# Kernel tuning notes

Hardware: AMD Instinct MI355X
Metric: run time of the kernel (lower is better)

Reference implementation:

```python
import jax, jax.numpy as jnp
import numpy as np

N_QUBITS = 12
N_LAYERS = 6
BATCH = 512
DIM = 2 ** N_QUBITS


def _apply_1q(psi, G, wire):
    """Apply a single-qubit gate on `wire` (wire 0 = most significant).
    psi: [B, 2^n] complex. G: [2,2] (shared) or [B,2,2] (batched)."""
    B = psi.shape[0]
    left = 2 ** wire
    psi = psi.reshape(B, left, 2, -1)
    if G.ndim == 2:
        psi = jnp.einsum('ij,bxjy->bxiy', G, psi)
    else:
        psi = jnp.einsum('bij,bxjy->bxiy', G, psi)
    return psi.reshape(B, -1)


def _apply_cnot(psi, c, t):
    """CNOT with control c, target t on [B, 2^n] state."""
    B = psi.shape[0]
    ps = psi.reshape((B,) + (2,) * N_QUBITS)
    ca, ta = c + 1, t + 1
    c0 = jnp.take(ps, 0, axis=ca)
    c1 = jnp.take(ps, 1, axis=ca)
    flip_ax = ta if ta < ca else ta - 1
    c1 = jnp.flip(c1, axis=flip_ax)  # X on target within control=1 block
    ps = jnp.stack([c0, c1], axis=ca)
    return ps.reshape(B, -1)


def _circuit(x, weights):
    B = x.shape[0]
    psi = jnp.zeros((B, DIM), jnp.complex64).at[:, 0].set(1.0)

    # AngleEmbedding: RY(x_w) on each wire (batched gate matrices)
    h = 0.5 * x
    c, s = jnp.cos(h).astype(jnp.complex64), jnp.sin(h).astype(jnp.complex64)
    for w in range(N_QUBITS):
        G = jnp.stack([jnp.stack([c[:, w], -s[:, w]], -1),
                       jnp.stack([s[:, w], c[:, w]], -1)], -2)  # [B,2,2]
        psi = _apply_1q(psi, G, w)

    # StronglyEntanglingLayers: Rot(phi,theta,omega) per wire, then ring of CNOTs
    for l in range(N_LAYERS):
        phi, theta, omega = weights[l, :, 0], weights[l, :, 1], weights[l, :, 2]
        ct = jnp.cos(0.5 * theta).astype(jnp.complex64)
        st = jnp.sin(0.5 * theta).astype(jnp.complex64)
        ep = jnp.exp(-0.5j * (phi + omega).astype(jnp.complex64))
        em = jnp.exp(0.5j * (phi - omega).astype(jnp.complex64))
        # Rot = RZ(omega) RY(theta) RZ(phi)
        m00 = ep * ct
        m01 = -em * st
        m10 = jnp.conj(em) * st
        m11 = jnp.conj(ep) * ct
        for w in range(N_QUBITS):
            G = jnp.array([[m00[w], m01[w]], [m10[w], m11[w]]], jnp.complex64)
            psi = _apply_1q(psi, G, w)
        r = l % (N_QUBITS - 1) + 1
        for w in range(N_QUBITS):
            psi = _apply_cnot(psi, w, (w + r) % N_QUBITS)

    # <Z_w> for every wire
    probs = psi.real ** 2 + psi.imag ** 2  # [B, 2^n]
    exps = []
    for w in range(N_QUBITS):
        p = probs.reshape(B, 2 ** w, 2, -1)
        exps.append(p[:, :, 0, :].sum((1, 2)) - p[:, :, 1, :].sum((1, 2)))
    return jnp.stack(exps, -1)  # [B, n_qubits]


def setup_inputs() -> dict:
    key = jax.random.key(0)
    k1, k2, k3, k4 = jax.random.split(key, 4)
    x = jax.random.uniform(k1, (BATCH, N_QUBITS), jnp.float32, -np.pi, np.pi)
    weights = jax.random.uniform(k2, (N_LAYERS, N_QUBITS, 3), jnp.float32, 0.0, 2.0 * np.pi)
    W = jax.random.normal(k3, (1, N_QUBITS), jnp.float32) * 0.3
    b = jax.random.normal(k4, (1,), jnp.float32) * 0.01
    return {"x": x, "weights": weights, "W": W, "b": b}


def reference(x, weights, W, b):
    z = _circuit(x, weights)              # [B, n_qubits]
    y = z @ W.T + b                       # [B, 1]
    return y.squeeze(-1)                  # [B]
```

## Files before the change

kernel.cpp:

```cpp
#include <hip/hip_runtime.h>
#include <stdint.h>

#define NQ 12
#define DIM 4096
#define NLAYERS 6
#define TPB 512
#define NL 8

typedef float v2f __attribute__((ext_vector_type(2)));

struct Pass_t {
    uint32_t WT[9];
    uint32_t WL[NL];
    uint32_t RT[9];
    uint32_t RL[NL];
};
struct CK_t {
    Pass_t PS1, PS2, PS3;
    Pass_t P1[NLAYERS];
    uint32_t frow[NQ];
};

constexpr uint32_t S1f(uint32_t k){ return ((k&7u)<<3) | ((k>>3)&7u) | (k & 0xFC0u); }
constexpr uint32_t S2f(uint32_t k){ return ((k&7u)<<6) | (k & 0x38u) | ((k>>6)&7u) | (k & 0xE00u); }
constexpr uint32_t S3f(uint32_t k){ return ((k&7u)<<9) | (k & 0x1F8u) | ((k>>9)&7u); }

constexpr uint32_t ech_reduce(const uint32_t* v, int n, uint32_t x){
    bool ch = true;
    while (ch) {
        ch = false;
        for (int i = 0; i < n; i++)
            if (v[i] && (x ^ v[i]) < x) { x ^= v[i]; ch = true; }
    }
    return x;
}

constexpr Pass_t build_pass(const uint32_t* Mc) {
    Pass_t P{};
    uint32_t rows[12]{}; int nr = 0;
    {
        uint32_t e1[4]{}, e2[4]{}; int n1 = 0, n2 = 0;
        for (int step = 0; step < 4; step++) {
            bool found = false;
            for (int pc = 1; pc <= 3 && !found; pc++) {
                for (int a = 0; a < 12 && !found; a++)
                for (int b = (pc >= 2 ? a + 1 : 12); (pc >= 2 ? b < 12 : b == 12) && !found; b++)
                for (int c = (pc == 3 ? b + 1 : 12); (pc == 3 ? c < 12 : c == 12) && !found; c++) {
                    uint32_t m = (1u << a);
                    if (pc >= 2) m |= (1u << b);
                    if (pc == 3) m |= (1u << c);
                    uint32_t v1 = (m >> 3) & 15u;
                    uint32_t v2 = 0;
                    for (int j = 0; j < 4; j++)
                        v2 |= (uint32_t)(__builtin_popcount(m & Mc[3 + j]) & 1) << j;
                    uint32_t r1 = ech_reduce(e1, n1, v1);
                    uint32_t r2 = ech_reduce(e2, n2, v2);
                    if (r1 && r2) {
                        rows[nr++] = m; e1[n1++] = r1; e2[n2++] = r2; found = true;
                    }
                }
            }
            if (!found) { rows[nr] = 1u << (3 + nr); nr++; }
        }
    }
    {
        uint32_t ef[12]{}; int nf = 0;
        for (int i = 0; i < nr; i++) {
            uint32_t r = ech_reduce(ef, nf, rows[i]);
            if (r) ef[nf++] = r;
        }
        for (uint32_t m = 1; m < 4096u && nr < 12; m++) {
            uint32_t r = ech_reduce(ef, nf, m);
            if (r) { rows[nr++] = m; ef[nf++] = r; }
        }
    }
    uint32_t col[12]{}, rc[12]{};
    for (int j = 0; j < 12; j++) {
        uint32_t c = 0;
        for (int i = 0; i < 12; i++) c |= (uint32_t)((rows[i] >> j) & 1u) << i;
        col[j] = c;
    }
    for (int j = 0; j < 12; j++) {
        uint32_t a = 0, mc = Mc[j];
        for (int q = 0; q < 12; q++) if ((mc >> q) & 1u) a ^= col[q];
        rc[j] = a;
    }
    for (int j = 0; j < 9; j++) { P.WT[j] = col[3 + j]; P.RT[j] = rc[3 + j]; }
    for (int l = 0; l < NL; l++) {
        uint32_t aw = 0, ar = 0;
        for (int q = 0; q < 3; q++) if ((l >> q) & 1) { aw ^= col[q]; ar ^= rc[q]; }
        P.WL[l] = aw; P.RL[l] = ar;
    }
    return P;
}

constexpr CK_t build_ck() {
    CK_t ck{};
    uint32_t Acols[NLAYERS][NQ]{}, Aicol5[NQ]{};
    for (int l = 0; l < NLAYERS; l++) {
        int r = l % (NQ - 1) + 1;
        for (int q = 0; q < NQ; q++) {
            uint32_t v = 1u << q;
            for (int w = NQ - 1; w >= 0; w--) {
                int pc = NQ - 1 - w, pt = NQ - 1 - ((w + r) % NQ);
                v ^= ((v >> pc) & 1u) << pt;
            }
            Acols[l][q] = v;
            if (l == NLAYERS - 1) {
                uint32_t u = 1u << q;
                for (int w = 0; w < NQ; w++) {
                    int pc = NQ - 1 - w, pt = NQ - 1 - ((w + r) % NQ);
                    u ^= ((u >> pc) & 1u) << pt;
                }
                Aicol5[q] = u;
            }
        }
    }
    uint32_t Mc[12]{};
    for (int j = 0; j < 12; j++) Mc[j] = S1f(1u << j);
    ck.PS1 = build_pass(Mc);
    for (int j = 0; j < 12; j++) Mc[j] = S2f(1u << j);
    ck.PS2 = build_pass(Mc);
    for (int j = 0; j < 12; j++) Mc[j] = S3f(1u << j);
    ck.PS3 = build_pass(Mc);
    for (int l = 1; l < NLAYERS; l++) {
        for (int j = 0; j < 12; j++) Mc[j] = S3f(S2f(S1f(Acols[l - 1][j])));
        ck.P1[l] = build_pass(Mc);
    }
    uint32_t Mcol[NQ]{};
    for (int j = 0; j < NQ; j++) {
        uint32_t pj = S1f(S2f(S3f(1u << j)));
        uint32_t M = 0;
        for (int m = 0; m < NQ; m++) if ((pj >> m) & 1u) M ^= Aicol5[m];
        Mcol[j] = M;
    }
    for (int p = 0; p < NQ; p++) {
        uint32_t s = 0;
        for (int j = 0; j < NQ; j++) s |= ((Mcol[j] >> p) & 1u) << j;
        ck.frow[p] = s;
    }
    return ck;
}
constexpr CK_t CK = build_ck();

template<int KIND, int L, int PAR>
__device__ __forceinline__ void do_pass(v2f (&Z)[NL], v2f* xb, int tid) {
    constexpr Pass_t P = (KIND == 1) ? CK.P1[L]
                       : (KIND == 2) ? CK.PS1
                       : (KIND == 3) ? CK.PS2 : CK.PS3;
    v2f* buf = xb + PAR * DIM;
    uint32_t comb = 0;
    #pragma unroll
    for (int j = 0; j < 9; j++) {
        uint32_t pk = P.WT[j] | (P.RT[j] << 16);
        comb ^= (uint32_t)(-(int)((tid >> j) & 1)) & pk;
    }
    uint32_t wbase = comb & 0xFFFu, rbase = comb >> 16;
    #pragma unroll
    for (int l = 0; l < NL; l++)
        buf[wbase ^ P.WL[l]] = Z[l];
    __syncthreads();
    #pragma unroll
    for (int l = 0; l < NL; l++)
        Z[l] = buf[rbase ^ P.RL[l]];
}

template<int L, int W, int Q>
__device__ __forceinline__ void reg_gate(v2f (&Z)[NL], const float4* smat) {
    float4 m = smat[L * NQ + W];
    #pragma unroll
    for (int l = 0; l < NL; l++) {
        if (l & (1 << Q)) continue;
        int l2 = l | (1 << Q);
        v2f z0 = Z[l], z1 = Z[l2];
        v2f j0 = { -z0.y, z0.x };
        v2f j1 = { -z1.y, z1.x };
        Z[l]  = m.x * z0 + m.y * j0 + m.z * z1 + m.w * j1;
        Z[l2] = m.x * z1 - m.y * j1 - m.z * z0 + m.w * j0;
    }
}

template<int L>
__device__ __forceinline__ void do_layer(v2f (&Z)[NL], const float4* smat,
                                         v2f* xb, int tid) {
    if constexpr (L > 0)
        do_pass<1, L, 1>(Z, xb, tid);
    reg_gate<L, 11, 0>(Z, smat);
    reg_gate<L, 10, 1>(Z, smat);
    reg_gate<L,  9, 2>(Z, smat);
    do_pass<2, L, 0>(Z, xb, tid);
    reg_gate<L, 8, 0>(Z, smat);
    reg_gate<L, 7, 1>(Z, smat);
    reg_gate<L, 6, 2>(Z, smat);
    do_pass<3, L, 1>(Z, xb, tid);
    reg_gate<L, 5, 0>(Z, smat);
    reg_gate<L, 4, 1>(Z, smat);
    reg_gate<L, 3, 2>(Z, smat);
    do_pass<4, L, 0>(Z, xb, tid);
    reg_gate<L, 2, 0>(Z, smat);
    reg_gate<L, 1, 1>(Z, smat);
    reg_gate<L, 0, 2>(Z, smat);
}

__global__ __launch_bounds__(TPB) void qsim_kernel(
    const float* __restrict__ x,
    const float* __restrict__ weights,
    const float* __restrict__ Wp,
    const float* __restrict__ bptr,
    float* __restrict__ out)
{
    __shared__ v2f    xb[2 * DIM];
    __shared__ float4 smat[NLAYERS * NQ];
    __shared__ float  scs[NQ], sss[NQ];
    __shared__ float  red[8];

    const int tid = threadIdx.x;
    const int b   = blockIdx.x;

    if (tid < NQ) {
        float s_, c_;
        sincosf(0.5f * x[b * NQ + tid], &s_, &c_);
        scs[tid] = c_; sss[tid] = s_;
    }
    if (tid < NLAYERS * NQ) {
        float phi   = weights[tid * 3 + 0];
        float theta = weights[tid * 3 + 1];
        float omega = weights[tid * 3 + 2];
        float st, ct; sincosf(0.5f * theta, &st, &ct);
        float sp, cp; sincosf(0.5f * (phi + omega), &sp, &cp);
        float sm, cm; sincosf(0.5f * (phi - omega), &sm, &cm);
        smat[tid] = make_float4(cp * ct, -sp * ct, -cm * st, -sm * st);
    }
    __syncthreads();

    float base = 1.0f;
    #pragma unroll
    for (int j = 0; j < 9; j++) {
        int w = 8 - j;
        base *= ((tid >> j) & 1) ? sss[w] : scs[w];
    }
    v2f Z[NL];
    #pragma unroll
    for (int l = 0; l < NL; l++) {
        float a = base;
        #pragma unroll
        for (int p = 0; p < 3; p++) {
            int w = NQ - 1 - p;
            a *= ((l >> p) & 1) ? sss[w] : scs[w];
        }
        Z[l].x = a; Z[l].y = 0.0f;
    }

    do_layer<0>(Z, smat, xb, tid);
    do_layer<1>(Z, smat, xb, tid);
    do_layer<2>(Z, smat, xb, tid);
    do_layer<3>(Z, smat, xb, tid);
    do_layer<4>(Z, smat, xb, tid);
    do_layer<5>(Z, smat, xb, tid);

    const float bv = bptr[0];
    float wb[NQ];
    #pragma unroll
    for (int p = 0; p < NQ; p++) {
        uint32_t row = CK.frow[p];
        int tp = __popc(tid & (int)(row >> 3)) & 1;
        float Wv = Wp[NQ - 1 - p];
        wb[p] = tp ? -Wv : Wv;
    }
    float acc = 0.0f;
    #pragma unroll
    for (int l = 0; l < NL; l++) {
        float coef = bv;
        #pragma unroll
        for (int p = 0; p < NQ; p++)
            coef += (__popc(l & (int)(CK.frow[p] & 7u)) & 1) ? -wb[p] : wb[p];
        acc += (Z[l].x * Z[l].x + Z[l].y * Z[l].y) * coef;
    }
    #pragma unroll
    for (int off = 32; off > 0; off >>= 1)
        acc += __shfl_down(acc, off, 64);
    if ((tid & 63) == 0) red[tid >> 6] = acc;
    __syncthreads();
    if (tid == 0) {
        float s = 0.0f;
        #pragma unroll
        for (int wv = 0; wv < TPB / 64; wv++) s += red[wv];
        out[b] = s;
    }
}

extern "C" void kernel_launch(void* const* d_in, const int* in_sizes, int n_in,
                              void* d_out, int out_size, void* d_ws, size_t ws_size,
                              hipStream_t stream) {
    const float* x       = (const float*)d_in[0];
    const float* weights = (const float*)d_in[1];
    const float* W       = (const float*)d_in[2];
    const float* bptr    = (const float*)d_in[3];
    qsim_kernel<<<512, TPB, 0, stream>>>(x, weights, W, bptr, (float*)d_out);
}
```

Baseline: 93.03 us.

## Pack two amplitudes per lane in split real/imag layout with packed FMA

Halves the block to 256 threads, with each thread now holding 16 amplitudes as paired real and imaginary vectors. The state is stored in LDS as separate real and imaginary planes, and the permutation matrices are rebuilt so one qubit bit is fixed across the packed pair. This lets gate math use packed two-wide FMAs and lets LDS accesses move 64-bit pairs where possible. The cost is more register pressure, fewer waves per block, and scalar LDS reads on passes where the pairing bit is not preserved.

```diff
diff --git a/kernel.cpp b/kernel.cpp
--- a/kernel.cpp
+++ b/kernel.cpp
@@ -4,16 +4,16 @@
 #define NQ 12
 #define DIM 4096
 #define NLAYERS 6
-#define TPB 512
-#define NL 8
+#define TPB 256
 
 typedef float v2f __attribute__((ext_vector_type(2)));
 
 struct Pass_t {
-    uint32_t WT[9];
-    uint32_t WL[NL];
-    uint32_t RT[9];
-    uint32_t RL[NL];
+    uint32_t WT[8];
+    uint32_t WL[8];
+    uint32_t RT[8];
+    uint32_t RL[16];
+    bool r64;
 };
 struct CK_t {
     Pass_t PS1, PS2, PS3;
@@ -37,44 +37,54 @@
 
 constexpr Pass_t build_pass(const uint32_t* Mc) {
     Pass_t P{};
-    uint32_t rows[12]{}; int nr = 0;
-    {
-        uint32_t e1[4]{}, e2[4]{}; int n1 = 0, n2 = 0;
-        for (int step = 0; step < 4; step++) {
-            bool found = false;
-            for (int pc = 1; pc <= 3 && !found; pc++) {
-                for (int a = 0; a < 12 && !found; a++)
-                for (int b = (pc >= 2 ? a + 1 : 12); (pc >= 2 ? b < 12 : b == 12) && !found; b++)
-                for (int c = (pc == 3 ? b + 1 : 12); (pc == 3 ? c < 12 : c == 12) && !found; c++) {
-                    uint32_t m = (1u << a);
-                    if (pc >= 2) m |= (1u << b);
-                    if (pc == 3) m |= (1u << c);
-                    uint32_t v1 = (m >> 3) & 15u;
-                    uint32_t v2 = 0;
-                    for (int j = 0; j < 4; j++)
-                        v2 |= (uint32_t)(__builtin_popcount(m & Mc[3 + j]) & 1) << j;
-                    uint32_t r1 = ech_reduce(e1, n1, v1);
-                    uint32_t r2 = ech_reduce(e2, n2, v2);
-                    if (r1 && r2) {
-                        rows[nr++] = m; e1[n1++] = r1; e2[n2++] = r2; found = true;
-                    }
-                }
+    bool r64 = (Mc[3] == 8u);
+    for (int j = 0; j < 12; j++) if (j != 3 && (Mc[j] & 8u)) r64 = false;
+    P.r64 = r64;
+
+    uint32_t rows[12]{};
+    rows[0] = 8u;
+    int nr = 1;
+    uint32_t full[12]{}; int nf = 0; full[nf++] = 8u;
+    uint32_t We[4]{};  int nw = 0;
+    uint32_t Re[5]{};  int nre = 0;
+    const int rpn = r64 ? 4 : 5;
+    if (!r64) {
+        uint32_t p0 = 0;
+        for (int j = 0; j < rpn; j++)
+            p0 |= (uint32_t)(__builtin_popcount(8u & Mc[4 + j]) & 1) << j;
+        uint32_t r = ech_reduce(Re, nre, p0);
+        if (r) Re[nre++] = r;
+    }
+    for (int slot = 0; slot < 4; slot++) {
+        uint32_t chosen = 0;
+        for (int relax = 0; relax < 3 && !chosen; relax++) {
+            for (uint32_t m = 1; m < 4096u && !chosen; m++) {
+                if (m & 8u) continue;
+                uint32_t wp = (m >> 4) & 15u;
+                uint32_t wr = ech_reduce(We, nw, wp);
+                if (relax < 2 && !wr) continue;
+                uint32_t rp = 0;
+                for (int j = 0; j < rpn; j++)
+                    rp |= (uint32_t)(__builtin_popcount(m & Mc[4 + j]) & 1) << j;
+                uint32_t rr = ech_reduce(Re, nre, rp);
+                if (relax < 1 && !rr) continue;
+                uint32_t fr = ech_reduce(full, nf, m);
+                if (!fr) continue;
+                chosen = m; full[nf++] = fr;
+                if (wr && nw < 4) We[nw++] = wr;
+                if (rr && nre < 5) Re[nre++] = rr;
             }
-            if (!found) { rows[nr] = 1u << (3 + nr); nr++; }
-        }
-    }
-    {
-        uint32_t ef[12]{}; int nf = 0;
-        for (int i = 0; i < nr; i++) {
-            uint32_t r = ech_reduce(ef, nf, rows[i]);
-            if (r) ef[nf++] = r;
-        }
-        for (uint32_t m = 1; m < 4096u && nr < 12; m++) {
-            uint32_t r = ech_reduce(ef, nf, m);
-            if (r) { rows[nr++] = m; ef[nf++] = r; }
-        }
-    }
-    uint32_t col[12]{}, rc[12]{};
+        }
+        rows[nr++] = chosen;
+    }
+    for (int slot = 5; slot < 12; slot++) {
+        for (uint32_t m = 1; m < 4096u; m++) {
+            if (m & 8u) continue;
+            uint32_t fr = ech_reduce(full, nf, m);
+            if (fr) { rows[nr++] = m; full[nf++] = fr; break; }
+        }
+    }
+    uint32_t col[12]{}, lmc[12]{};
     for (int j = 0; j < 12; j++) {
         uint32_t c = 0;
         for (int i = 0; i < 12; i++) c |= (uint32_t)((rows[i] >> j) & 1u) << i;
@@ -83,13 +93,18 @@
     for (int j = 0; j < 12; j++) {
         uint32_t a = 0, mc = Mc[j];
         for (int q = 0; q < 12; q++) if ((mc >> q) & 1u) a ^= col[q];
-        rc[j] = a;
-    }
-    for (int j = 0; j < 9; j++) { P.WT[j] = col[3 + j]; P.RT[j] = rc[3 + j]; }
-    for (int l = 0; l < NL; l++) {
-        uint32_t aw = 0, ar = 0;
-        for (int q = 0; q < 3; q++) if ((l >> q) & 1) { aw ^= col[q]; ar ^= rc[q]; }
-        P.WL[l] = aw; P.RL[l] = ar;
+        lmc[j] = a;
+    }
+    for (int j = 0; j < 8; j++) { P.WT[j] = col[4 + j]; P.RT[j] = lmc[4 + j]; }
+    for (int j = 0; j < 8; j++) {
+        uint32_t a = 0;
+        for (int q = 0; q < 3; q++) if ((j >> q) & 1) a ^= col[q];
+        P.WL[j] = a;
+    }
+    for (int l = 0; l < 16; l++) {
+        uint32_t a = 0;
+        for (int q = 0; q < 4; q++) if ((l >> q) & 1) a ^= lmc[q];
+        P.RL[l] = a;
     }
     return P;
 }
@@ -144,62 +159,93 @@
 constexpr CK_t CK = build_ck();
 
 template<int KIND, int L, int PAR>
-__device__ __forceinline__ void do_pass(v2f (&Z)[NL], v2f* xb, int tid) {
+__device__ __forceinline__ void do_pass(v2f (&PRE)[8], v2f (&PIM)[8],
+                                        float* lds, int tid) {
     constexpr Pass_t P = (KIND == 1) ? CK.P1[L]
                        : (KIND == 2) ? CK.PS1
                        : (KIND == 3) ? CK.PS2 : CK.PS3;
-    v2f* buf = xb + PAR * DIM;
+    float* buf = lds + PAR * (2 * DIM);
     uint32_t comb = 0;
     #pragma unroll
-    for (int j = 0; j < 9; j++) {
+    for (int j = 0; j < 8; j++) {
         uint32_t pk = P.WT[j] | (P.RT[j] << 16);
         comb ^= (uint32_t)(-(int)((tid >> j) & 1)) & pk;
     }
-    uint32_t wbase = comb & 0xFFFu, rbase = comb >> 16;
-    #pragma unroll
-    for (int l = 0; l < NL; l++)
-        buf[wbase ^ P.WL[l]] = Z[l];
+    uint32_t wb = comb & 0xFFFFu, rb = comb >> 16;
+    v2f* bre = (v2f*)buf;
+    v2f* bim = (v2f*)(buf + DIM);
+    #pragma unroll
+    for (int j = 0; j < 8; j++) {
+        uint32_t s = (wb ^ P.WL[j]) >> 1;
+        bre[s] = PRE[j];
+        bim[s] = PIM[j];
+    }
     __syncthreads();
-    #pragma unroll
-    for (int l = 0; l < NL; l++)
-        Z[l] = buf[rbase ^ P.RL[l]];
+    if constexpr (P.r64) {
+        #pragma unroll
+        for (int j = 0; j < 8; j++) {
+            uint32_t s = (rb ^ P.RL[j]) >> 1;
+            PRE[j] = bre[s];
+            PIM[j] = bim[s];
+        }
+    } else {
+        #pragma unroll
+        for (int j = 0; j < 8; j++) {
+            uint32_t s0 = rb ^ P.RL[j], s1 = rb ^ P.RL[j | 8];
+            v2f re, im;
+            re.x = buf[s0];        re.y = buf[s1];
+            im.x = buf[DIM + s0];  im.y = buf[DIM + s1];
+            PRE[j] = re;
+            PIM[j] = im;
+        }
+    }
 }
 
 template<int L, int W, int Q>
-__device__ __forceinline__ void reg_gate(v2f (&Z)[NL], const float4* smat) {
+__device__ __forceinline__ void reg_gate(v2f (&PRE)[8], v2f (&PIM)[8],
+                                         const float4* smat) {
     float4 m = smat[L * NQ + W];
-    #pragma unroll
-    for (int l = 0; l < NL; l++) {
-        if (l & (1 << Q)) continue;
-        int l2 = l | (1 << Q);
-        v2f z0 = Z[l], z1 = Z[l2];
-        v2f j0 = { -z0.y, z0.x };
-        v2f j1 = { -z1.y, z1.x };
-        Z[l]  = m.x * z0 + m.y * j0 + m.z * z1 + m.w * j1;
-        Z[l2] = m.x * z1 - m.y * j1 - m.z * z0 + m.w * j0;
+    v2f bx = {m.x, m.x}, by = {m.y, m.y}, bz = {m.z, m.z}, bw = {m.w, m.w};
+    #pragma unroll
+    for (int j = 0; j < 8; j++) {
+        if (j & (1 << Q)) continue;
+        int j2 = j | (1 << Q);
+        v2f re0 = PRE[j], im0 = PIM[j], re1 = PRE[j2], im1 = PIM[j2];
+        PRE[j]  = __builtin_elementwise_fma(bx, re0,
+                  __builtin_elementwise_fma(by, -im0,
+                  __builtin_elementwise_fma(bz, re1, -bw * im1)));
+        PIM[j]  = __builtin_elementwise_fma(bx, im0,
+                  __builtin_elementwise_fma(by, re0,
+                  __builtin_elementwise_fma(bz, im1, bw * re1)));
+        PRE[j2] = __builtin_elementwise_fma(bx, re1,
+                  __builtin_elementwise_fma(by, im1,
+                  __builtin_elementwise_fma(bz, -re0, -bw * im0)));
+        PIM[j2] = __builtin_elementwise_fma(bx, im1,
+                  __builtin_elementwise_fma(by, -re1,
+                  __builtin_elementwise_fma(bz, -im0, bw * re0)));
     }
 }
 
 template<int L>
-__device__ __forceinline__ void do_layer(v2f (&Z)[NL], const float4* smat,
-                                         v2f* xb, int tid) {
+__device__ __forceinline__ void do_layer(v2f (&PRE)[8], v2f (&PIM)[8],
+                                         const float4* smat, float* lds, int tid) {
     if constexpr (L > 0)
-        do_pass<1, L, 1>(Z, xb, tid);
-    reg_gate<L, 11, 0>(Z, smat);
-    reg_gate<L, 10, 1>(Z, smat);
-    reg_gate<L,  9, 2>(Z, smat);
-    do_pass<2, L, 0>(Z, xb, tid);
-    reg_gate<L, 8, 0>(Z, smat);
-    reg_gate<L, 7, 1>(Z, smat);
-    reg_gate<L, 6, 2>(Z, smat);
-    do_pass<3, L, 1>(Z, xb, tid);
-    reg_gate<L, 5, 0>(Z, smat);
-    reg_gate<L, 4, 1>(Z, smat);
-    reg_gate<L, 3, 2>(Z, smat);
-    do_pass<4, L, 0>(Z, xb, tid);
-    reg_gate<L, 2, 0>(Z, smat);
-    reg_gate<L, 1, 1>(Z, smat);
-    reg_gate<L, 0, 2>(Z, smat);
+        do_pass<1, L, 1>(PRE, PIM, lds, tid);
+    reg_gate<L, 11, 0>(PRE, PIM, smat);
+    reg_gate<L, 10, 1>(PRE, PIM, smat);
+    reg_gate<L,  9, 2>(PRE, PIM, smat);
+    do_pass<2, L, 0>(PRE, PIM, lds, tid);
+    reg_gate<L, 8, 0>(PRE, PIM, smat);
+    reg_gate<L, 7, 1>(PRE, PIM, smat);
+    reg_gate<L, 6, 2>(PRE, PIM, smat);
+    do_pass<3, L, 1>(PRE, PIM, lds, tid);
+    reg_gate<L, 5, 0>(PRE, PIM, smat);
+    reg_gate<L, 4, 1>(PRE, PIM, smat);
+    reg_gate<L, 3, 2>(PRE, PIM, smat);
+    do_pass<4, L, 0>(PRE, PIM, lds, tid);
+    reg_gate<L, 2, 0>(PRE, PIM, smat);
+    reg_gate<L, 1, 1>(PRE, PIM, smat);
+    reg_gate<L, 0, 2>(PRE, PIM, smat);
 }
 
 __global__ __launch_bounds__(TPB) void qsim_kernel(
@@ -209,10 +255,10 @@
     const float* __restrict__ bptr,
     float* __restrict__ out)
 {
-    __shared__ v2f    xb[2 * DIM];
+    __shared__ float  lds[2 * 2 * DIM];
     __shared__ float4 smat[NLAYERS * NQ];
     __shared__ float  scs[NQ], sss[NQ];
-    __shared__ float  red[8];
+    __shared__ float  red[4];
 
     const int tid = threadIdx.x;
     const int b   = blockIdx.x;
@@ -235,58 +281,61 @@
 
     float base = 1.0f;
     #pragma unroll
-    for (int j = 0; j < 9; j++) {
-        int w = 8 - j;
+    for (int j = 0; j < 8; j++) {
+        int w = 7 - j;
         base *= ((tid >> j) & 1) ? sss[w] : scs[w];
     }
-    v2f Z[NL];
-    #pragma unroll
-    for (int l = 0; l < NL; l++) {
+    v2f PRE[8], PIM[8];
+    float c8 = scs[8], s8 = sss[8];
+    #pragma unroll
+    for (int j = 0; j < 8; j++) {
         float a = base;
         #pragma unroll
         for (int p = 0; p < 3; p++) {
             int w = NQ - 1 - p;
-            a *= ((l >> p) & 1) ? sss[w] : scs[w];
-        }
-        Z[l].x = a; Z[l].y = 0.0f;
-    }
-
-    do_layer<0>(Z, smat, xb, tid);
-    do_layer<1>(Z, smat, xb, tid);
-    do_layer<2>(Z, smat, xb, tid);
-    do_layer<3>(Z, smat, xb, tid);
-    do_layer<4>(Z, smat, xb, tid);
-    do_layer<5>(Z, smat, xb, tid);
+            a *= ((j >> p) & 1) ? sss[w] : scs[w];
+        }
+        PRE[j].x = a * c8;  PRE[j].y = a * s8;
+        PIM[j].x = 0.0f;    PIM[j].y = 0.0f;
+    }
+
+    do_layer<0>(PRE, PIM, smat, lds, tid);
+    do_layer<1>(PRE, PIM, smat, lds, tid);
+    do_layer<2>(PRE, PIM, smat, lds, tid);
+    do_layer<3>(PRE, PIM, smat, lds, tid);
+    do_layer<4>(PRE, PIM, smat, lds, tid);
+    do_layer<5>(PRE, PIM, smat, lds, tid);
 
     const float bv = bptr[0];
-    float wb[NQ];
+    float wbT[NQ];
     #pragma unroll
     for (int p = 0; p < NQ; p++) {
         uint32_t row = CK.frow[p];
-        int tp = __popc(tid & (int)(row >> 3)) & 1;
+        int tp = __popc(tid & (int)(row >> 4)) & 1;
         float Wv = Wp[NQ - 1 - p];
-        wb[p] = tp ? -Wv : Wv;
-    }
-    float acc = 0.0f;
-    #pragma unroll
-    for (int l = 0; l < NL; l++) {
-        float coef = bv;
+        wbT[p] = tp ? -Wv : Wv;
+    }
+    v2f acc2 = {0.0f, 0.0f};
+    #pragma unroll
+    for (int j = 0; j < 8; j++) {
+        float cx = bv, cy = bv;
         #pragma unroll
-        for (int p = 0; p < NQ; p++)
-            coef += (__popc(l & (int)(CK.frow[p] & 7u)) & 1) ? -wb[p] : wb[p];
-        acc += (Z[l].x * Z[l].x + Z[l].y * Z[l].y) * coef;
-    }
+        for (int p = 0; p < NQ; p++) {
+            uint32_t row = CK.frow[p];
+            float s = (__popc(j & (int)(row & 7u)) & 1) ? -wbT[p] : wbT[p];
+            cx += s;
+            cy += (row & 8u) ? -s : s;
+        }
+        v2f c = {cx, cy};
+        acc2 += (PRE[j] * PRE[j] + PIM[j] * PIM[j]) * c;
+    }
+    float acc = acc2.x + acc2.y;
     #pragma unroll
     for (int off = 32; off > 0; off >>= 1)
         acc += __shfl_down(acc, off, 64);
     if ((tid & 63) == 0) red[tid >> 6] = acc;
     __syncthreads();
-    if (tid == 0) {
-        float s = 0.0f;
-        #pragma unroll
-        for (int wv = 0; wv < TPB / 64; wv++) s += red[wv];
-        out[b] = s;
-    }
+    if (tid == 0) out[b] = red[0] + red[1] + red[2] + red[3];
 }
 
 extern "C" void kernel_launch(void* const* d_in, const int* in_sizes, int n_in,
```

After: 91.80 us. Within noise of the previous version (-1.3%).
